# Optimization experiments

Hardware: AMD Instinct MI355X
Metric: run time of the kernel (lower is better)

Reference implementation:

```python
import jax, jax.numpy as jnp
import numpy as np

NSTEPS = 64  # Euler integration steps for the CPAB ODE solve


def cpab_basis_1d(nC):
    """Null-space basis of the continuity constraints for a 1D CPAB
    tessellation with nC cells (velocity a_c*x + b_c per cell, continuous
    at interior knots, no zero-boundary constraint). Returns [2*nC, nC+1]."""
    d = 2 * nC
    L = np.zeros((nC - 1, d), dtype=np.float64)
    for k in range(1, nC):  # small fixed loop over cells
        xk = k / nC
        L[k - 1, 2 * (k - 1):2 * k] = [xk, 1.0]
        L[k - 1, 2 * k:2 * k + 2] = [-xk, -1.0]
    _, _, Vt = np.linalg.svd(L)
    return np.ascontiguousarray(Vt[nC - 1:].T).astype(np.float32)  # [2nC, nC+1]


def setup_inputs() -> dict:
    key = jax.random.key(0)
    k1, k2 = jax.random.split(key)
    B, Lin, C, nC = 256, 2048, 32, 32
    x = jax.random.normal(k1, (B, Lin, C), dtype=jnp.float32)
    theta = 0.5 * jax.random.normal(k2, (B, nC + 1), dtype=jnp.float32)
    basis = jnp.asarray(cpab_basis_1d(nC))  # [64, 33]
    return {"x": x, "theta": theta, "basis": basis, "out_len": 2048}


def reference(x, theta, basis, out_len):
    # x: [B, Lin, C]; theta: [B, d]; basis: [2*nC, d]
    B, Lin, C = x.shape
    nC = basis.shape[0] // 2
    dt = 1.0 / NSTEPS

    # Per-cell affine velocity coefficients: v_c(x) = a_c * x + b_c
    A = jnp.einsum('kd,bd->bk', basis, theta).reshape(B, nC, 2)
    Aa, Ab = A[..., 0], A[..., 1]  # each [B, nC]

    # Integrate dphi/dt = v(phi) from the uniform grid on [0,1]
    grid = jnp.linspace(0.0, 1.0, out_len, dtype=x.dtype)
    phi0 = jnp.broadcast_to(grid, (B, out_len))

    def step(phi, _):
        idx = jnp.clip(jnp.floor(phi * nC).astype(jnp.int32), 0, nC - 1)
        a = jnp.take_along_axis(Aa, idx, axis=1)
        b = jnp.take_along_axis(Ab, idx, axis=1)
        return phi + (a * phi + b) * dt, None

    phi, _ = jax.lax.scan(step, phi0, None, length=NSTEPS)

    # Linear resampling of x at the warped grid
    p = jnp.clip(phi, 0.0, 1.0) * (Lin - 1)           # [B, out_len]
    i0 = jnp.clip(jnp.floor(p).astype(jnp.int32), 0, Lin - 2)
    w = (p - i0.astype(p.dtype))[..., None]           # [B, out_len, 1]
    g0 = jnp.take_along_axis(x, i0[..., None], axis=1)        # [B, out_len, C]
    g1 = jnp.take_along_axis(x, (i0 + 1)[..., None], axis=1)  # [B, out_len, C]
    return g0 * (1.0 - w) + g1 * w
```

## Files before the change

kernel.cpp:

```cpp
#include <hip/hip_runtime.h>


#define NSTEPS 64
#define NC     32
#define DD     33
#define LIN    2048
#define CCH    32
#define OUTLEN 2048
#define JPW    64
#define WPB    4
#define JPB    (JPW * WPB)

typedef const __attribute__((address_space(1))) void gvoid_t;
typedef __attribute__((address_space(3))) void svoid_t;
typedef float f32x4 __attribute__((ext_vector_type(4)));

__global__ __launch_bounds__(256) void cpab_warp_kernel(
    const float* __restrict__ x,
    const float* __restrict__ theta,
    const float* __restrict__ basis,
    float* __restrict__ out)
{
    __shared__ float2 ctab[WPB][NC];
    __shared__ float2 iw[WPB][JPW];
    __shared__ float  pfs[WPB][256];

    const int t    = threadIdx.x;
    const int wave = t >> 6;
    const int lane = t & 63;
    const int blocksPerB = OUTLEN / JPB;
    const int b      = blockIdx.x / blocksPerB;
    const int blockJ = (blockIdx.x % blocksPerB) * JPB;
    const int jbase  = blockJ + wave * JPW;

    const float dt = 1.0f / (float)NSTEPS;

    {
        const char* src = (const char*)(x + ((size_t)b * LIN + blockJ + wave * JPW) * CCH)
                          + lane * 16;
        svoid_t* dst = (svoid_t*)&pfs[wave][0];
        #pragma unroll
        for (int k = 0; k < 8; ++k) {
            __builtin_amdgcn_global_load_lds((gvoid_t*)(src + (size_t)k * 1024), dst, 16, 0, 0);
        }
    }

    float acc = 0.0f;
    {
        const float* bs = basis + lane * DD;
        const float* th = theta + b * DD;
        #pragma unroll
        for (int d = 0; d < DD; ++d) acc = fmaf(bs[d], th[d], acc);
    }
    {
        int c = lane & (NC - 1);
        float a  = __shfl(acc, 2 * c);
        float bb = __shfl(acc, 2 * c + 1);
        if (lane < NC) ctab[wave][c] = make_float2(fmaf(a, dt, 1.0f), bb * dt);
    }

    {
        const int j = jbase + lane;
        float phi = (float)j * (1.0f / (float)(OUTLEN - 1));
        const float2* ct = ctab[wave];
        #pragma unroll
        for (int s = 0; s < NSTEPS; ++s) {
            float f = fminf(fmaxf(phi * (float)NC, 0.0f), (float)(NC - 1));
            float2 cc = ct[(int)f];
            phi = fmaf(cc.x, phi, cc.y);
        }
        float p = fminf(fmaxf(phi, 0.0f), 1.0f) * (float)(LIN - 1);
        int i0 = min(max((int)p, 0), LIN - 2);
        iw[wave][lane] = make_float2(p - (float)i0, (float)i0);
    }

    const f32x4* xb = (const f32x4*)(x + (size_t)b * (LIN * CCH));
    f32x4* ob = (f32x4*)(out + ((size_t)b * OUTLEN + jbase) * CCH);
    const int c4  = lane & 7;
    const int jl0 = lane >> 3;

    float2 f[8];
    #pragma unroll
    for (int it = 0; it < 8; ++it) f[it] = iw[wave][it * 8 + jl0];

    #pragma unroll
    for (int it = 0; it < 8; ++it) {
        int   jl = it * 8 + jl0;
        int   i0 = (int)f[it].y;
        float w  = f[it].x;
        f32x4 g0 = xb[i0 * (CCH / 4) + c4];
        f32x4 g1 = xb[(i0 + 1) * (CCH / 4) + c4];
        f32x4 r = g0 + w * (g1 - g0);
        __builtin_nontemporal_store(r, &ob[jl * (CCH / 4) + c4]);
    }
}

extern "C" void kernel_launch(void* const* d_in, const int* in_sizes, int n_in,
                              void* d_out, int out_size, void* d_ws, size_t ws_size,
                              hipStream_t stream) {
    const float* x     = (const float*)d_in[0];
    const float* theta = (const float*)d_in[1];
    const float* basis = (const float*)d_in[2];
    float* out = (float*)d_out;

    const int B = in_sizes[1] / DD;
    const int grid = B * (OUTLEN / JPB);
    cpab_warp_kernel<<<grid, 256, 0, stream>>>(x, theta, basis, out);
}
```

Before: 32.23 us.

## Split ODE integration and gather into two kernels via workspace

Splits the fused kernel in two. The first kernel integrates the ODE and writes warped positions to the workspace. The second kernel reads those positions and does the bilinear gather of x. The change also drops the unused global_load_lds prefetch of x into LDS and replaces the nontemporal stores with plain stores. The intent is to decouple the latency-bound ODE loop from the memory-bound gather, which adds a second launch and a round trip of positions through global memory.

```diff
diff --git a/kernel.cpp b/kernel.cpp
--- a/kernel.cpp
+++ b/kernel.cpp
@@ -11,39 +11,23 @@
 #define WPB    4
 #define JPB    (JPW * WPB)
 
-typedef const __attribute__((address_space(1))) void gvoid_t;
-typedef __attribute__((address_space(3))) void svoid_t;
 typedef float f32x4 __attribute__((ext_vector_type(4)));
 
-__global__ __launch_bounds__(256) void cpab_warp_kernel(
-    const float* __restrict__ x,
+__global__ __launch_bounds__(256) void cpab_ode_kernel(
     const float* __restrict__ theta,
     const float* __restrict__ basis,
-    float* __restrict__ out)
+    float* __restrict__ pws)
 {
     __shared__ float2 ctab[WPB][NC];
-    __shared__ float2 iw[WPB][JPW];
-    __shared__ float  pfs[WPB][256];
 
     const int t    = threadIdx.x;
     const int wave = t >> 6;
     const int lane = t & 63;
     const int blocksPerB = OUTLEN / JPB;
-    const int b      = blockIdx.x / blocksPerB;
-    const int blockJ = (blockIdx.x % blocksPerB) * JPB;
-    const int jbase  = blockJ + wave * JPW;
+    const int b = blockIdx.x / blocksPerB;
+    const int j = (blockIdx.x % blocksPerB) * JPB + wave * JPW + lane;
 
     const float dt = 1.0f / (float)NSTEPS;
-
-    {
-        const char* src = (const char*)(x + ((size_t)b * LIN + blockJ + wave * JPW) * CCH)
-                          + lane * 16;
-        svoid_t* dst = (svoid_t*)&pfs[wave][0];
-        #pragma unroll
-        for (int k = 0; k < 8; ++k) {
-            __builtin_amdgcn_global_load_lds((gvoid_t*)(src + (size_t)k * 1024), dst, 16, 0, 0);
-        }
-    }
 
     float acc = 0.0f;
     {
@@ -59,6 +43,79 @@
         if (lane < NC) ctab[wave][c] = make_float2(fmaf(a, dt, 1.0f), bb * dt);
     }
 
+    float phi = (float)j * (1.0f / (float)(OUTLEN - 1));
+    const float2* ct = ctab[wave];
+    #pragma unroll
+    for (int s = 0; s < NSTEPS; ++s) {
+        float f = fminf(fmaxf(phi * (float)NC, 0.0f), (float)(NC - 1));
+        float2 cc = ct[(int)f];
+        phi = fmaf(cc.x, phi, cc.y);
+    }
+    pws[b * OUTLEN + j] = fminf(fmaxf(phi, 0.0f), 1.0f) * (float)(LIN - 1);
+}
+
+__global__ __launch_bounds__(256) void cpab_gather_kernel(
+    const float* __restrict__ x,
+    const float* __restrict__ pws,
+    float* __restrict__ out)
+{
+    const int t    = threadIdx.x;
+    const int wave = t >> 6;
+    const int lane = t & 63;
+    const int blocksPerB = OUTLEN / JPB;
+    const int b     = blockIdx.x / blocksPerB;
+    const int jbase = (blockIdx.x % blocksPerB) * JPB + wave * JPW;
+
+    const f32x4* xb = (const f32x4*)(x + (size_t)b * (LIN * CCH));
+    f32x4* ob = (f32x4*)(out + ((size_t)b * OUTLEN + jbase) * CCH);
+    const float* pw = pws + b * OUTLEN + jbase;
+    const int c4  = lane & 7;
+    const int jl0 = lane >> 3;
+
+    float p[8];
+    #pragma unroll
+    for (int it = 0; it < 8; ++it) p[it] = pw[it * 8 + jl0];
+
+    #pragma unroll
+    for (int it = 0; it < 8; ++it) {
+        int   i0 = min((int)p[it], LIN - 2);
+        float w  = p[it] - (float)i0;
+        f32x4 g0 = xb[i0 * (CCH / 4) + c4];
+        f32x4 g1 = xb[(i0 + 1) * (CCH / 4) + c4];
+        ob[(it * 8 + jl0) * (CCH / 4) + c4] = g0 + w * (g1 - g0);
+    }
+}
+
+__global__ __launch_bounds__(256) void cpab_fused_kernel(
+    const float* __restrict__ x,
+    const float* __restrict__ theta,
+    const float* __restrict__ basis,
+    float* __restrict__ out)
+{
+    __shared__ float2 ctab[WPB][NC];
+    __shared__ float2 iw[WPB][JPW];
+
+    const int t    = threadIdx.x;
+    const int wave = t >> 6;
+    const int lane = t & 63;
+    const int blocksPerB = OUTLEN / JPB;
+    const int b     = blockIdx.x / blocksPerB;
+    const int jbase = (blockIdx.x % blocksPerB) * JPB + wave * JPW;
+    const float dt = 1.0f / (float)NSTEPS;
+
+    float acc = 0.0f;
+    {
+        const float* bs = basis + lane * DD;
+        const float* th = theta + b * DD;
+        #pragma unroll
+        for (int d = 0; d < DD; ++d) acc = fmaf(bs[d], th[d], acc);
+    }
+    {
+        int c = lane & (NC - 1);
+        float a  = __shfl(acc, 2 * c);
+        float bb = __shfl(acc, 2 * c + 1);
+        if (lane < NC) ctab[wave][c] = make_float2(fmaf(a, dt, 1.0f), bb * dt);
+    }
     {
         const int j = jbase + lane;
         float phi = (float)j * (1.0f / (float)(OUTLEN - 1));
@@ -73,25 +130,20 @@
         int i0 = min(max((int)p, 0), LIN - 2);
         iw[wave][lane] = make_float2(p - (float)i0, (float)i0);
     }
-
     const f32x4* xb = (const f32x4*)(x + (size_t)b * (LIN * CCH));
     f32x4* ob = (f32x4*)(out + ((size_t)b * OUTLEN + jbase) * CCH);
     const int c4  = lane & 7;
     const int jl0 = lane >> 3;
-
     float2 f[8];
     #pragma unroll
     for (int it = 0; it < 8; ++it) f[it] = iw[wave][it * 8 + jl0];
-
     #pragma unroll
     for (int it = 0; it < 8; ++it) {
-        int   jl = it * 8 + jl0;
         int   i0 = (int)f[it].y;
         float w  = f[it].x;
         f32x4 g0 = xb[i0 * (CCH / 4) + c4];
         f32x4 g1 = xb[(i0 + 1) * (CCH / 4) + c4];
-        f32x4 r = g0 + w * (g1 - g0);
-        __builtin_nontemporal_store(r, &ob[jl * (CCH / 4) + c4]);
+        ob[(it * 8 + jl0) * (CCH / 4) + c4] = g0 + w * (g1 - g0);
     }
 }
 
@@ -105,5 +157,13 @@
 
     const int B = in_sizes[1] / DD;
     const int grid = B * (OUTLEN / JPB);
-    cpab_warp_kernel<<<grid, 256, 0, stream>>>(x, theta, basis, out);
+    const size_t need = (size_t)B * OUTLEN * sizeof(float);
+
+    if (ws_size >= need) {
+        float* pws = (float*)d_ws;
+        cpab_ode_kernel<<<grid, 256, 0, stream>>>(theta, basis, pws);
+        cpab_gather_kernel<<<grid, 256, 0, stream>>>(x, pws, out);
+    } else {
+        cpab_fused_kernel<<<grid, 256, 0, stream>>>(x, theta, basis, out);
+    }
 }
```

Result: slower. 37.28 us (+15.7%).
